# Optimization experiments

Hardware: AMD Instinct MI355X
Metric: run time of the kernel (lower is better)

## Reference

```python
import jax, jax.numpy as jnp
import numpy as np

B, S, HID = 1, 2048, 2048
NH, NKV, D = 32, 4, 128   # query heads, kv heads, head_dim
ROPE_THETA = 1e6
EPS = 1e-6


def _rms_norm(x, w):
    # per-head RMSNorm over head_dim, computed in fp32 (Qwen3MoeRMSNorm)
    xf = x.astype(jnp.float32)
    var = jnp.mean(xf * xf, axis=-1, keepdims=True)
    return (w * (xf * jax.lax.rsqrt(var + EPS))).astype(x.dtype)


def _rotate_half(x):
    x1, x2 = jnp.split(x, 2, axis=-1)
    return jnp.concatenate([-x2, x1], axis=-1)


def setup_inputs() -> dict:
    key = jax.random.key(0)
    ks = jax.random.split(key, 5)
    hidden_states = jax.random.normal(ks[0], (B, S, HID), jnp.float32)
    # weights stored as (in, out); torch Linear computes x @ W.T with W (out,in) -- same math
    wq = jax.random.normal(ks[1], (HID, NH * D), jnp.float32) * 0.02
    wk = jax.random.normal(ks[2], (HID, NKV * D), jnp.float32) * 0.02
    wv = jax.random.normal(ks[3], (HID, NKV * D), jnp.float32) * 0.02
    wo = jax.random.normal(ks[4], (NH * D, HID), jnp.float32) * 0.02
    q_norm_w = jnp.ones((D,), jnp.float32)
    k_norm_w = jnp.ones((D,), jnp.float32)
    # RoPE tables (rotate_half convention, like HF Qwen3)
    inv_freq = 1.0 / (ROPE_THETA ** (jnp.arange(0, D, 2, dtype=jnp.float32) / D))
    freqs = jnp.arange(S, dtype=jnp.float32)[:, None] * inv_freq[None, :]  # [S, D/2]
    emb = jnp.concatenate([freqs, freqs], axis=-1)  # [S, D]
    cos, sin = jnp.cos(emb), jnp.sin(emb)
    # causal mask (True = keep)
    attention_mask = jnp.tril(jnp.ones((S, S), bool))[None, None]
    return {
        'hidden_states': hidden_states, 'cos': cos, 'sin': sin,
        'wq': wq, 'wk': wk, 'wv': wv, 'wo': wo,
        'q_norm_w': q_norm_w, 'k_norm_w': k_norm_w,
        'attention_mask': attention_mask, 'start_pos': 0,
    }


def reference(hidden_states, cos, sin, wq, wk, wv, wo, q_norm_w, k_norm_w,
              attention_mask, start_pos):
    b, s, _ = hidden_states.shape
    # projections + per-head RMSNorm, then [B, H, S, D]
    q = _rms_norm((hidden_states @ wq).reshape(b, s, NH, D), q_norm_w).transpose(0, 2, 1, 3)
    k = _rms_norm((hidden_states @ wk).reshape(b, s, NKV, D), k_norm_w).transpose(0, 2, 1, 3)
    v = (hidden_states @ wv).reshape(b, s, NKV, D).transpose(0, 2, 1, 3)
    # rotary embedding (rotate_half form); start_pos=0 -> tables already aligned
    c = cos[None, None, :, :]
    sn = sin[None, None, :, :]
    q = q * c + _rotate_half(q) * sn
    k = k * c + _rotate_half(k) * sn
    # GQA: repeat kv heads to match query heads
    groups = NH // NKV
    k = jnp.repeat(k, groups, axis=1)
    v = jnp.repeat(v, groups, axis=1)
    scaling = D ** -0.5
    scores = jnp.einsum('bhqd,bhkd->bhqk', q, k) * scaling  # [B, NH, S, S]
    scores = jnp.where(attention_mask, scores, jnp.float32(-1e9))
    attn = jax.nn.softmax(scores, axis=-1)
    out = jnp.einsum('bhqk,bhkd->bhqd', attn, v)  # [B, NH, S, D]
    out = out.transpose(0, 2, 1, 3).reshape(b, s, NH * D)
    return out @ wo
```

## Files before the change

kernel.cpp:

```cpp
#include <hip/hip_runtime.h>
#include <hip/hip_bf16.h>

using short4v = __attribute__((ext_vector_type(4))) short;
using short8 = __attribute__((ext_vector_type(8))) short;
using f32x4  = __attribute__((ext_vector_type(4))) float;

#define SEQ 2048
#define NHEAD 32
#define NKVH 4
#define HDIM 128
#define QK_SCALE_LOG2 (0.08838834764831845f * 1.44269504088896340f)

__device__ __forceinline__ float fast_exp2(float x) { return __builtin_amdgcn_exp2f(x); }
__device__ __forceinline__ float b2f(short u) {
    return __uint_as_float(((unsigned)(unsigned short)u) << 16);
}
__device__ __forceinline__ short f2bb(float f) {
    __hip_bfloat16 h = __float2bfloat16(f);
    return *reinterpret_cast<short*>(&h);
}
__device__ __forceinline__ void gload_lds16(const __hip_bfloat16* src, __hip_bfloat16* dst) {
    __builtin_amdgcn_global_load_lds((const __attribute__((address_space(1))) void*)src,
                                     (__attribute__((address_space(3))) void*)dst, 16, 0, 0);
}

__global__ __launch_bounds__(256) void prep_kernel(
    const float* __restrict__ hs, __hip_bfloat16* __restrict__ hsb,
    const float* __restrict__ wq, const float* __restrict__ wk, const float* __restrict__ wv,
    const float* __restrict__ wo,
    __hip_bfloat16* __restrict__ WqkvT, __hip_bfloat16* __restrict__ WoT) {
    const int b = blockIdx.x, tid = threadIdx.x;
    if (b < 4096) {
        int i = b * 256 + tid;
        float4 v = ((const float4*)hs)[i];
        __hip_bfloat16 h4[4] = {__float2bfloat16(v.x), __float2bfloat16(v.y),
                                __float2bfloat16(v.z), __float2bfloat16(v.w)};
        ((ushort4*)hsb)[i] = *(ushort4*)h4;
        return;
    }
    __shared__ float tile[32][33];
    const float* W; __hip_bfloat16* Wt; int N, ld, nb, kb;
    if (b < 12288)      { int bb = b - 4096;  W = wq; Wt = WqkvT;                       N = 4096; ld = 2048; nb = (bb & 127) * 32; kb = (bb >> 7) * 32; }
    else if (b < 13312) { int bb = b - 12288; W = wk; Wt = WqkvT + (size_t)4096 * 2048; N = 512;  ld = 2048; nb = (bb & 15) * 32;  kb = (bb >> 4) * 32; }
    else if (b < 14336) { int bb = b - 13312; W = wv; Wt = WqkvT + (size_t)4608 * 2048; N = 512;  ld = 2048; nb = (bb & 15) * 32;  kb = (bb >> 4) * 32; }
    else                { int bb = b - 14336; W = wo; Wt = WoT;                         N = 2048; ld = 4096; nb = (bb & 63) * 32;  kb = (bb >> 6) * 32; }
    int tx = tid & 31, ty = tid >> 5;
    for (int j = 0; j < 32; j += 8)
        tile[ty + j][tx] = W[(size_t)(kb + ty + j) * N + nb + tx];
    __syncthreads();
    for (int j = 0; j < 32; j += 8)
        Wt[(size_t)(nb + ty + j) * ld + kb + tx] = __float2bfloat16(tile[tx][ty + j]);
}

__global__ void add3b_kernel(const __hip_bfloat16* __restrict__ a, const __hip_bfloat16* __restrict__ b,
                             const __hip_bfloat16* __restrict__ c, float* __restrict__ o, int n4) {
    int i = blockIdx.x * blockDim.x + threadIdx.x;
    if (i >= n4) return;
    short4v x = ((const short4v*)a)[i];
    short4v y = ((const short4v*)b)[i];
    short4v z = ((const short4v*)c)[i];
    float4 r = {b2f(x[0]) + b2f(y[0]) + b2f(z[0]), b2f(x[1]) + b2f(y[1]) + b2f(z[1]),
                b2f(x[2]) + b2f(y[2]) + b2f(z[2]), b2f(x[3]) + b2f(y[3]) + b2f(z[3])};
    ((float4*)o)[i] = r;
}

#define BM 128
#define BN 128
#define BK2 64
template <typename OutT>
__global__ __launch_bounds__(256) void gemm_bt_kernel(
    const __hip_bfloat16* __restrict__ A, const __hip_bfloat16* __restrict__ Bt,
    OutT* __restrict__ C, int M, int N, int KextMax, int ld, int koff, long long czstride, int Ktot) {
    const int kstart = blockIdx.z * koff;
    const int Kext = min(KextMax, Ktot - kstart);
    A  += (size_t)kstart;
    Bt += (size_t)kstart;
    C  += (size_t)blockIdx.z * czstride;
    __shared__ __align__(16) __hip_bfloat16 sA[BM * BK2];
    __shared__ __align__(16) __hip_bfloat16 sB[BN * BK2];
    const int tid = threadIdx.x;
    const int w = tid >> 6, l = tid & 63;
    const int wr = w >> 1, wc = w & 1;
    const int row0 = blockIdx.y * BM;
    const int col0 = blockIdx.x * BN;
    const int fr = l & 15;
    const int fq = l >> 4;
    const int xs = (fr & 7) << 4;

    f32x4 acc[4][4] = {};

    for (int k0 = 0; k0 < Kext; k0 += BK2) {
        for (int i = 0; i < 4; ++i) {
            int ch = i * 256 + tid;
            int row = ch >> 3;
            int cb = ((ch & 7) * 16) ^ ((row & 7) << 4);
            gload_lds16(A  + (size_t)(row0 + row) * ld + k0 + (cb >> 1), &sA[ch * 8]);
            gload_lds16(Bt + (size_t)(col0 + row) * ld + k0 + (cb >> 1), &sB[ch * 8]);
        }
        __syncthreads();
        short8 af[4][2], bfr[4][2];
        for (int m = 0; m < 4; ++m) {
            const char* base = (const char*)sA + (wr * 64 + m * 16 + fr) * 128;
            af[m][0] = *(const short8*)(base + (((fq) * 16)     ^ xs));
            af[m][1] = *(const short8*)(base + (((fq + 4) * 16) ^ xs));
        }
        for (int n = 0; n < 4; ++n) {
            const char* base = (const char*)sB + (wc * 64 + n * 16 + fr) * 128;
            bfr[n][0] = *(const short8*)(base + (((fq) * 16)     ^ xs));
            bfr[n][1] = *(const short8*)(base + (((fq + 4) * 16) ^ xs));
        }
        for (int kk = 0; kk < 2; ++kk)
            for (int m = 0; m < 4; ++m)
                for (int n = 0; n < 4; ++n)
                    acc[m][n] = __builtin_amdgcn_mfma_f32_16x16x32_bf16(af[m][kk], bfr[n][kk], acc[m][n], 0, 0, 0);
        __syncthreads();
    }
    for (int m = 0; m < 4; ++m)
        for (int n = 0; n < 4; ++n)
            for (int r = 0; r < 4; ++r) {
                int row = row0 + wr * 64 + m * 16 + fq * 4 + r;
                int col = col0 + wc * 64 + n * 16 + fr;
                float v = acc[m][n][r];
                if constexpr (__is_same(OutT, float)) C[(size_t)row * N + col] = v;
                else C[(size_t)row * N + col] = __float2bfloat16(v);
            }
}

__global__ __launch_bounds__(256) void pack_kernel(
    const __hip_bfloat16* __restrict__ P0, const __hip_bfloat16* __restrict__ P1,
    const float* __restrict__ cosp, const float* __restrict__ sinp,
    const float* __restrict__ qnw, const float* __restrict__ knw,
    __hip_bfloat16* __restrict__ Qh, __hip_bfloat16* __restrict__ Kh, __hip_bfloat16* __restrict__ Vt) {
    const int tid = threadIdx.x;
    const int rloc = tid >> 4, l16 = tid & 15;
    const int r = blockIdx.y * 16 + rloc;
    const int s = blockIdx.x * 2 + (r >= 40 ? 1 : 0);
    const int slot = (r >= 40) ? r - 40 : r;
    int off;
    if (slot < 32)      off = slot * 128;
    else if (slot < 36) off = 4096 + (slot - 32) * 128;
    else                off = 4608 + (slot - 36) * 128;
    const int d0 = l16 * 4;
    const size_t base = (size_t)s * 5120 + off;

    short4v a0 = *(const short4v*)&P0[base + d0];
    short4v a1 = *(const short4v*)&P0[base + d0 + 64];
    short4v b0 = *(const short4v*)&P1[base + d0];
    short4v b1 = *(const short4v*)&P1[base + d0 + 64];
    float x1[4], x2[4];
    for (int j = 0; j < 4; ++j) {
        x1[j] = b2f(a0[j]) + b2f(b0[j]);
        x2[j] = b2f(a1[j]) + b2f(b1[j]);
    }

    if (slot >= 36) {
        int t = slot - 36;
        for (int j = 0; j < 4; ++j) {
            Vt[((size_t)t * 128 + d0 + j) * SEQ + s]      = __float2bfloat16(x1[j]);
            Vt[((size_t)t * 128 + d0 + 64 + j) * SEQ + s] = __float2bfloat16(x2[j]);
        }
        return;
    }
    float ss = 0.f;
    for (int j = 0; j < 4; ++j) ss += x1[j] * x1[j] + x2[j] * x2[j];
    for (int x = 1; x < 16; x <<= 1) ss += __shfl_xor(ss, x);
    float rs = rsqrtf(ss * (1.0f / 128.0f) + 1e-6f);

    f32x4 c4 = *(const f32x4*)&cosp[(size_t)s * 128 + d0];
    f32x4 s4 = *(const f32x4*)&sinp[(size_t)s * 128 + d0];
    const float* wgt = (slot < 32) ? qnw : knw;
    f32x4 w1 = *(const f32x4*)&wgt[d0];
    f32x4 w2 = *(const f32x4*)&wgt[d0 + 64];
    const float scl = (slot < 32) ? QK_SCALE_LOG2 : 1.0f;

    short4v o1, o2;
    for (int j = 0; j < 4; ++j) {
        float a = x1[j] * rs * w1[j], b = x2[j] * rs * w2[j];
        o1[j] = f2bb((a * c4[j] - b * s4[j]) * scl);
        o2[j] = f2bb((b * c4[j] + a * s4[j]) * scl);
    }
    __hip_bfloat16* dst;
    if (slot < 32) dst = Qh + ((size_t)slot * SEQ + s) * 128;
    else           dst = Kh + ((size_t)(slot - 32) * SEQ + s) * 128;
    *(short4v*)&dst[d0]      = o1;
    *(short4v*)&dst[d0 + 64] = o2;
}

__global__ __launch_bounds__(256, 2) void attn_kernel(
    const __hip_bfloat16* __restrict__ Qh,
    const __hip_bfloat16* __restrict__ Kh,
    const __hip_bfloat16* __restrict__ Vt,
    __hip_bfloat16* __restrict__ Oa) {
    __shared__ __align__(16) __hip_bfloat16 sK[2][64 * 128];
    __shared__ __align__(16) __hip_bfloat16 sV[2][128 * 64];
    __shared__ __align__(16) __hip_bfloat16 sP[4][16 * 72];

    const int tid = threadIdx.x;
    const int w = tid >> 6, l = tid & 63;
    const int bx = blockIdx.x;
    const int y = bx & 7;
    const int qt = 127 - (bx >> 3);
    const int qbase = qt * 16;
    const int hkv = y >> 1;
    const int h = y * 4 + w;
    const int fr = l & 15, g = l >> 4;

    const __hip_bfloat16* Qp = Qh + ((size_t)h * SEQ + qbase) * HDIM;
    const __hip_bfloat16* Kp = Kh + (size_t)hkv * SEQ * HDIM;
    const __hip_bfloat16* Vp = Vt + (size_t)hkv * HDIM * SEQ;
    __hip_bfloat16* myP = &sP[w][0];

    short8 qf[4];
    for (int c = 0; c < 4; ++c)
        qf[c] = *(const short8*)&Qp[fr * HDIM + c * 32 + g * 8];

    f32x4 oacc[8] = {};
    float m_s = -3.0e38f;
    float l_s = 0.f;

    const int xr = (fr & 7) << 4;
    const int qg = qbase + fr;
    const int ntiles = ((qbase + 15) >> 6) + 1;

    auto stage = [&](int buf, int kbase) {
        for (int i = 0; i < 4; ++i) {
            int blk = i * 4 + w;
            {
                int row = blk * 4 + (l >> 4);
                int cb = ((l & 15) * 16) ^ ((row & 7) << 4);
                gload_lds16(Kp + (size_t)(kbase + row) * HDIM + (cb >> 1), &sK[buf][blk * 512]);
            }
            {
                int row = blk * 8 + (l >> 3);
                int cb = ((l & 7) * 16) ^ ((row & 7) << 4);
                gload_lds16(Vp + (size_t)row * SEQ + kbase + (cb >> 1), &sV[buf][blk * 512]);
            }
        }
    };

    stage(0, 0);
    __syncthreads();

    for (int t = 0; t < ntiles; ++t) {
        const int kbase = t * 64;
        const int buf = t & 1;
        if (t + 1 < ntiles) stage(buf ^ 1, kbase + 64);

        f32x4 s[4] = {};
        __builtin_amdgcn_s_setprio(1);
        for (int j = 0; j < 4; ++j) {
            const __hip_bfloat16* kp = &sK[buf][(j * 16 + fr) * 128];
            for (int c = 0; c < 4; ++c) {
                short8 kf = *(const short8*)&kp[((c * 64 + g * 16) ^ xr) >> 1];
                s[j] = __builtin_amdgcn_mfma_f32_16x16x32_bf16(kf, qf[c], s[j], 0, 0, 0);
            }
        }
        __builtin_amdgcn_s_setprio(0);

        float v[4][4];
        const bool full = (kbase + 63 <= qbase);
        if (full) {
            for (int j = 0; j < 4; ++j)
                for (int r = 0; r < 4; ++r) v[j][r] = s[j][r];
        } else {
            const int kb0 = kbase + g * 4;
            for (int j = 0; j < 4; ++j)
                for (int r = 0; r < 4; ++r)
                    v[j][r] = (kb0 + j * 16 + r <= qg) ? s[j][r] : -1e30f;
        }
        float m0 = fmaxf(fmaxf(v[0][0], v[0][1]), fmaxf(v[0][2], v[0][3]));
        float m1 = fmaxf(fmaxf(v[1][0], v[1][1]), fmaxf(v[1][2], v[1][3]));
        float m2 = fmaxf(fmaxf(v[2][0], v[2][1]), fmaxf(v[2][2], v[2][3]));
        float m3 = fmaxf(fmaxf(v[3][0], v[3][1]), fmaxf(v[3][2], v[3][3]));
        float m = fmaxf(fmaxf(m0, m1), fmaxf(m2, m3));
        m = fmaxf(m, __shfl_xor(m, 16));
        m = fmaxf(m, __shfl_xor(m, 32));
        if (__any(m > m_s + 12.0f)) {
            float mnew = fmaxf(m_s, m);
            float corr = fast_exp2(m_s - mnew);
            m_s = mnew;
            l_s *= corr;
            float c0 = __shfl(corr, g * 4 + 0);
            float c1 = __shfl(corr, g * 4 + 1);
            float c2 = __shfl(corr, g * 4 + 2);
            float c3 = __shfl(corr, g * 4 + 3);
            for (int dt = 0; dt < 8; ++dt) {
                oacc[dt][0] *= c0; oacc[dt][1] *= c1;
                oacc[dt][2] *= c2; oacc[dt][3] *= c3;
            }
        }
        for (int j = 0; j < 4; ++j) {
            float e0 = fast_exp2(v[j][0] - m_s);
            float e1 = fast_exp2(v[j][1] - m_s);
            float e2 = fast_exp2(v[j][2] - m_s);
            float e3 = fast_exp2(v[j][3] - m_s);
            l_s += (e0 + e1) + (e2 + e3);
            short4v pw = {f2bb(e0), f2bb(e1), f2bb(e2), f2bb(e3)};
            *(short4v*)((char*)myP + fr * 144 + j * 32 + g * 8) = pw;
        }
        short8 pa0 = *(const short8*)&myP[fr * 72 + g * 8];
        short8 pa1 = *(const short8*)&myP[fr * 72 + 32 + g * 8];
        __builtin_amdgcn_s_setprio(1);
        for (int dt = 0; dt < 8; ++dt) {
            const __hip_bfloat16* vp = &sV[buf][(dt * 16 + fr) * 64];
            short8 vb0 = *(const short8*)&vp[((g * 16)      ^ xr) >> 1];
            short8 vb1 = *(const short8*)&vp[((g * 16 + 64) ^ xr) >> 1];
            oacc[dt] = __builtin_amdgcn_mfma_f32_16x16x32_bf16(pa0, vb0, oacc[dt], 0, 0, 0);
            oacc[dt] = __builtin_amdgcn_mfma_f32_16x16x32_bf16(pa1, vb1, oacc[dt], 0, 0, 0);
        }
        __builtin_amdgcn_s_setprio(0);
        __syncthreads();
    }

    l_s += __shfl_xor(l_s, 16);
    l_s += __shfl_xor(l_s, 32);
    float inv[4];
    for (int r = 0; r < 4; ++r)
        inv[r] = 1.0f / __shfl(l_s, g * 4 + r);
    for (int dt = 0; dt < 8; ++dt)
        for (int r = 0; r < 4; ++r) {
            int qq = qbase + g * 4 + r;
            Oa[(size_t)qq * (NHEAD * HDIM) + h * HDIM + dt * 16 + fr] =
                __float2bfloat16(oacc[dt][r] * inv[r]);
        }
}

extern "C" void kernel_launch(void* const* d_in, const int* in_sizes, int n_in,
                              void* d_out, int out_size, void* d_ws, size_t ws_size,
                              hipStream_t stream) {
    const float* hs   = (const float*)d_in[0];
    const float* cosp = (const float*)d_in[1];
    const float* sinp = (const float*)d_in[2];
    const float* wq   = (const float*)d_in[3];
    const float* wk   = (const float*)d_in[4];
    const float* wv   = (const float*)d_in[5];
    const float* wo   = (const float*)d_in[6];
    const float* qnw  = (const float*)d_in[7];
    const float* knw  = (const float*)d_in[8];
    float* out = (float*)d_out;
    char* ws = (char*)d_ws;

    __hip_bfloat16* hsb    = (__hip_bfloat16*)(ws);
    __hip_bfloat16* WqkvT  = (__hip_bfloat16*)(ws + 8388608);
    __hip_bfloat16* WoT    = (__hip_bfloat16*)(ws + 29360128);
    __hip_bfloat16* P0     = (__hip_bfloat16*)(ws + 46137344);
    __hip_bfloat16* P1     = (__hip_bfloat16*)(ws + 67108864);
    __hip_bfloat16* Qh     = (__hip_bfloat16*)(ws + 8388608);
    __hip_bfloat16* Kh     = (__hip_bfloat16*)(ws + 25165824);
    __hip_bfloat16* Vt     = (__hip_bfloat16*)(ws + 27262976);
    __hip_bfloat16* Oa     = (__hip_bfloat16*)(ws + 46137344);
    __hip_bfloat16* Qb     = (__hip_bfloat16*)(ws);

    prep_kernel<<<22528, 256, 0, stream>>>(hs, hsb, wq, wk, wv, wo, WqkvT, WoT);
    gemm_bt_kernel<__hip_bfloat16><<<dim3(40, 16, 2), 256, 0, stream>>>(
        hsb, WqkvT, P0, 2048, 5120, 1024, 2048, 1024, 10485760LL, 2048);
    pack_kernel<<<dim3(1024, 5), 256, 0, stream>>>(P0, P1, cosp, sinp, qnw, knw, Qh, Kh, Vt);
    attn_kernel<<<dim3(1024), 256, 0, stream>>>(Qh, Kh, Vt, Oa);
    gemm_bt_kernel<__hip_bfloat16><<<dim3(16, 16, 3), 256, 0, stream>>>(
        Oa, WoT, Qb, 2048, 2048, 1408, 4096, 1408, 4194304LL, 4096);
    add3b_kernel<<<4096, 256, 0, stream>>>(Qb, Qb + 4194304, Qb + 8388608, out, (2048 * 2048) / 4);
}
```

Baseline: 209.4 us.

## Store LDS tiles in MFMA fragment order instead of XOR-swizzled rows

Changes the shared-memory layout of the GEMM A/B tiles, the attention K/V tiles and the P scratch buffer so that each lane's 16-byte MFMA operand sits at a contiguous lane-indexed address. Fragment reads become simple l*16 offsets with no XOR swizzle arithmetic, and the padded P buffer shrinks. The global loads now gather 16-row fragment groups, so each wave's global accesses are scattered across rows in 64-byte pieces rather than spanning contiguous row segments, which may reduce global load efficiency.

```diff
diff --git a/kernel.cpp b/kernel.cpp
--- a/kernel.cpp
+++ b/kernel.cpp
@@ -79,35 +79,32 @@
     __shared__ __align__(16) __hip_bfloat16 sA[BM * BK2];
     __shared__ __align__(16) __hip_bfloat16 sB[BN * BK2];
     const int tid = threadIdx.x;
-    const int w = tid >> 6, l = tid & 63;
-    const int wr = w >> 1, wc = w & 1;
+    const int l = tid & 63;
+    const int wr = (tid >> 6) >> 1, wc = (tid >> 6) & 1;
     const int row0 = blockIdx.y * BM;
     const int col0 = blockIdx.x * BN;
     const int fr = l & 15;
     const int fq = l >> 4;
-    const int xs = (fr & 7) << 4;
 
     f32x4 acc[4][4] = {};
 
     for (int k0 = 0; k0 < Kext; k0 += BK2) {
         for (int i = 0; i < 4; ++i) {
-            int ch = i * 256 + tid;
-            int row = ch >> 3;
-            int cb = ((ch & 7) * 16) ^ ((row & 7) << 4);
-            gload_lds16(A  + (size_t)(row0 + row) * ld + k0 + (cb >> 1), &sA[ch * 8]);
-            gload_lds16(Bt + (size_t)(col0 + row) * ld + k0 + (cb >> 1), &sB[ch * 8]);
+            int chb = i * 256 + (tid & 192);
+            int ch = chb + l;
+            int rb = ch >> 7, kk = (ch >> 6) & 1, fq2 = (ch >> 4) & 3, fr2 = ch & 15;
+            gload_lds16(A  + (size_t)(row0 + rb * 16 + fr2) * ld + k0 + kk * 32 + fq2 * 8, &sA[chb * 8]);
+            gload_lds16(Bt + (size_t)(col0 + rb * 16 + fr2) * ld + k0 + kk * 32 + fq2 * 8, &sB[chb * 8]);
         }
         __syncthreads();
         short8 af[4][2], bfr[4][2];
         for (int m = 0; m < 4; ++m) {
-            const char* base = (const char*)sA + (wr * 64 + m * 16 + fr) * 128;
-            af[m][0] = *(const short8*)(base + (((fq) * 16)     ^ xs));
-            af[m][1] = *(const short8*)(base + (((fq + 4) * 16) ^ xs));
+            af[m][0] = *(const short8*)&sA[(((wr * 4 + m) * 2 + 0) * 64 + l) * 8];
+            af[m][1] = *(const short8*)&sA[(((wr * 4 + m) * 2 + 1) * 64 + l) * 8];
         }
         for (int n = 0; n < 4; ++n) {
-            const char* base = (const char*)sB + (wc * 64 + n * 16 + fr) * 128;
-            bfr[n][0] = *(const short8*)(base + (((fq) * 16)     ^ xs));
-            bfr[n][1] = *(const short8*)(base + (((fq + 4) * 16) ^ xs));
+            bfr[n][0] = *(const short8*)&sB[(((wc * 4 + n) * 2 + 0) * 64 + l) * 8];
+            bfr[n][1] = *(const short8*)&sB[(((wc * 4 + n) * 2 + 1) * 64 + l) * 8];
         }
         for (int kk = 0; kk < 2; ++kk)
             for (int m = 0; m < 4; ++m)
@@ -193,7 +190,7 @@
     __hip_bfloat16* __restrict__ Oa) {
     __shared__ __align__(16) __hip_bfloat16 sK[2][64 * 128];
     __shared__ __align__(16) __hip_bfloat16 sV[2][128 * 64];
-    __shared__ __align__(16) __hip_bfloat16 sP[4][16 * 72];
+    __shared__ __align__(16) __hip_bfloat16 sP[4][16 * 64];
 
     const int tid = threadIdx.x;
     const int w = tid >> 6, l = tid & 63;
@@ -208,7 +205,7 @@
     const __hip_bfloat16* Qp = Qh + ((size_t)h * SEQ + qbase) * HDIM;
     const __hip_bfloat16* Kp = Kh + (size_t)hkv * SEQ * HDIM;
     const __hip_bfloat16* Vp = Vt + (size_t)hkv * HDIM * SEQ;
-    __hip_bfloat16* myP = &sP[w][0];
+    char* myP = (char*)&sP[w][0];
 
     short8 qf[4];
     for (int c = 0; c < 4; ++c)
@@ -218,23 +215,20 @@
     float m_s = -3.0e38f;
     float l_s = 0.f;
 
-    const int xr = (fr & 7) << 4;
     const int qg = qbase + fr;
     const int ntiles = ((qbase + 15) >> 6) + 1;
 
     auto stage = [&](int buf, int kbase) {
         for (int i = 0; i < 4; ++i) {
-            int blk = i * 4 + w;
-            {
-                int row = blk * 4 + (l >> 4);
-                int cb = ((l & 15) * 16) ^ ((row & 7) << 4);
-                gload_lds16(Kp + (size_t)(kbase + row) * HDIM + (cb >> 1), &sK[buf][blk * 512]);
-            }
-            {
-                int row = blk * 8 + (l >> 3);
-                int cb = ((l & 7) * 16) ^ ((row & 7) << 4);
-                gload_lds16(Vp + (size_t)row * SEQ + kbase + (cb >> 1), &sV[buf][blk * 512]);
-            }
+            int chb = i * 256 + (tid & 192);
+            int ch = chb + l;
+            int g2 = (ch >> 4) & 3, fr2 = ch & 15;
+            gload_lds16(Kp + (size_t)(kbase + (ch >> 8) * 16 + fr2) * HDIM
+                           + ((ch >> 6) & 3) * 32 + g2 * 8,
+                        &sK[buf][chb * 8]);
+            gload_lds16(Vp + (size_t)((ch >> 7) * 16 + fr2) * SEQ + kbase
+                           + ((ch >> 6) & 1) * 32 + g2 * 8,
+                        &sV[buf][chb * 8]);
         }
     };
 
@@ -248,13 +242,11 @@
 
         f32x4 s[4] = {};
         __builtin_amdgcn_s_setprio(1);
-        for (int j = 0; j < 4; ++j) {
-            const __hip_bfloat16* kp = &sK[buf][(j * 16 + fr) * 128];
+        for (int j = 0; j < 4; ++j)
             for (int c = 0; c < 4; ++c) {
-                short8 kf = *(const short8*)&kp[((c * 64 + g * 16) ^ xr) >> 1];
+                short8 kf = *(const short8*)&sK[buf][((j * 4 + c) * 64 + l) * 8];
                 s[j] = __builtin_amdgcn_mfma_f32_16x16x32_bf16(kf, qf[c], s[j], 0, 0, 0);
             }
-        }
         __builtin_amdgcn_s_setprio(0);
 
         float v[4][4];
@@ -296,15 +288,16 @@
             float e3 = fast_exp2(v[j][3] - m_s);
             l_s += (e0 + e1) + (e2 + e3);
             short4v pw = {f2bb(e0), f2bb(e1), f2bb(e2), f2bb(e3)};
-            *(short4v*)((char*)myP + fr * 144 + j * 32 + g * 8) = pw;
-        }
-        short8 pa0 = *(const short8*)&myP[fr * 72 + g * 8];
-        short8 pa1 = *(const short8*)&myP[fr * 72 + 32 + g * 8];
+            *(short4v*)(myP + (j >> 1) * 1024
+                            + (((j & 1) * 2 + (g >> 1)) * 16 + fr) * 16
+                            + (g & 1) * 8) = pw;
+        }
+        short8 pa0 = *(const short8*)(myP + l * 16);
+        short8 pa1 = *(const short8*)(myP + 1024 + l * 16);
         __builtin_amdgcn_s_setprio(1);
         for (int dt = 0; dt < 8; ++dt) {
-            const __hip_bfloat16* vp = &sV[buf][(dt * 16 + fr) * 64];
-            short8 vb0 = *(const short8*)&vp[((g * 16)      ^ xr) >> 1];
-            short8 vb1 = *(const short8*)&vp[((g * 16 + 64) ^ xr) >> 1];
+            short8 vb0 = *(const short8*)&sV[buf][((dt * 2 + 0) * 64 + l) * 8];
+            short8 vb1 = *(const short8*)&sV[buf][((dt * 2 + 1) * 64 + l) * 8];
             oacc[dt] = __builtin_amdgcn_mfma_f32_16x16x32_bf16(pa0, vb0, oacc[dt], 0, 0, 0);
             oacc[dt] = __builtin_amdgcn_mfma_f32_16x16x32_bf16(pa1, vb1, oacc[dt], 0, 0, 0);
         }
```

New measurement: 296.3 us. 41.5% more time.
